# Kernel tuning notes

Measured on AMD Instinct MI355X. Metric: run time of the kernel, lower is better.

Reference implementation:

```python
import jax, jax.numpy as jnp
import numpy as np
from jax import lax

VOCAB, E, H = 32000, 256, 512
B, T = 64, 1024


def setup_inputs() -> dict:
    key = jax.random.key(0)
    ks = jax.random.split(key, 5)
    tokens = jax.random.randint(ks[0], (B, T), 0, VOCAB, dtype=jnp.int64 if jax.config.jax_enable_x64 else jnp.int32).astype(jnp.int32)
    emb_table = jax.random.normal(ks[1], (VOCAB, E), dtype=jnp.float32) * 0.02
    W_x = jax.random.normal(ks[2], (E, 4 * H), dtype=jnp.float32) * 0.02
    W_h = jax.random.normal(ks[3], (H, 4 * H), dtype=jnp.float32) * 0.02
    b = jnp.zeros((4 * H,), dtype=jnp.float32)
    h0 = jnp.zeros((B, H), dtype=jnp.float32)
    c0 = jnp.zeros((B, H), dtype=jnp.float32)
    return {"tokens": tokens, "h0": h0, "c0": c0, "emb_table": emb_table,
            "W_x": W_x, "W_h": W_h, "b": b}


def reference(tokens, h0, c0, emb_table, W_x, W_h, b):
    # Embedding lookup with mask_zero=True semantics: token 0 is padding.
    x = emb_table[tokens]                      # [B, T, E]
    mask = tokens != 0                         # [B, T]
    # Precompute input projections for all timesteps (same math, one GEMM).
    xz = jnp.einsum('bte,ef->btf', x, W_x) + b  # [B, T, 4H]

    def step(carry, inp):
        h, c = carry
        xzt, mt = inp                          # [B,4H], [B]
        z = xzt + h @ W_h                      # [B, 4H]
        i, f, g, o = jnp.split(z, 4, axis=-1)  # Keras gate order: i, f, c, o
        i = jax.nn.sigmoid(i)
        f = jax.nn.sigmoid(f)
        g = jnp.tanh(g)
        o = jax.nn.sigmoid(o)
        c_new = f * c + i * g
        h_new = o * jnp.tanh(c_new)
        m = mt[:, None]
        # Masked steps carry previous state/output (Keras masking behavior).
        h = jnp.where(m, h_new, h)
        c = jnp.where(m, c_new, c)
        return (h, c), h

    (h_T, c_T), outs = lax.scan(step, (h0, c0),
                                (xz.transpose(1, 0, 2), mask.T))
    return outs.transpose(1, 0, 2), h_T, c_T  # [B,T,H], [B,H], [B,H]
```

## Files before the change

kernel.cpp:

```cpp
#include <hip/hip_runtime.h>
#include <hip/hip_bf16.h>

#define B_ 64
#define T_ 1024
#define E_ 256
#define H_ 512
#define ZN_ 2048
#define NSLICE 64
#define KTX 8
#define KTH 16
#define KT_ (KTX + KTH)

typedef short bf16x8 __attribute__((ext_vector_type(8)));
typedef float f32x4 __attribute__((ext_vector_type(4)));
typedef int i32x4 __attribute__((ext_vector_type(4)));

union frag_u { i32x4 i; bf16x8 h; };

#define RAW_BAR() __builtin_amdgcn_s_barrier()
#define LGKM0() asm volatile("s_waitcnt lgkmcnt(0)" ::: "memory")
#define VM0() asm volatile("s_waitcnt vmcnt(0)" ::: "memory")

__device__ __forceinline__ short f2bf(float f) {
  union { float f; unsigned u; } v; v.f = f;
  unsigned r = v.u + 0x7fffu + ((v.u >> 16) & 1u);
  return (short)(r >> 16);
}
__device__ __forceinline__ float sigmoidf_(float x) { return 1.f / (1.f + __expf(-x)); }
__device__ __forceinline__ float tanhf_(float x) {
  x = fminf(10.f, fmaxf(-10.f, x));
  float e = __expf(2.f * x);
  return (e - 1.f) / (e + 1.f);
}

__device__ __forceinline__ i32x4 ld_sys(const void* p) {
  i32x4 r;
  asm volatile("global_load_dwordx4 %0, %1, off sc0 sc1" : "=v"(r) : "v"(p) : "memory");
  return r;
}
__device__ __forceinline__ void st_sys(void* p, i32x4 v) {
  asm volatile("global_store_dwordx4 %0, %1, off sc0 sc1" :: "v"(p), "v"(v) : "memory");
}
__device__ __forceinline__ int ld_sys_poll(const int* p) {
  int r;
  asm volatile("global_load_dword %0, %1, off sc0 sc1\n\ts_waitcnt vmcnt(0)"
               : "=v"(r) : "v"(p) : "memory");
  return r;
}
__device__ __forceinline__ void st_sys_i32(int* p, int v) {
  asm volatile("global_store_dword %0, %1, off sc0 sc1" :: "v"(p), "v"(v) : "memory");
}


__global__ void k_emb_cvt(const float* __restrict__ emb, short* __restrict__ dst, int n8) {
  int i = blockIdx.x * blockDim.x + threadIdx.x;
  if (i >= n8) return;
  const float4* s = (const float4*)emb;
  float4 a = s[2 * i], b = s[2 * i + 1];
  bf16x8 o;
  o[0] = f2bf(a.x); o[1] = f2bf(a.y); o[2] = f2bf(a.z); o[3] = f2bf(a.w);
  o[4] = f2bf(b.x); o[5] = f2bf(b.y); o[6] = f2bf(b.z); o[7] = f2bf(b.w);
  ((bf16x8*)dst)[i] = o;
}

__global__ void k_wfrag(const float* __restrict__ Wx, const float* __restrict__ Wh,
                        short* __restrict__ wf) {
  int tid = blockIdx.x * blockDim.x + threadIdx.x;
  if (tid >= NSLICE * 2 * KT_ * 64) return;
  int lane = tid & 63;
  int kt = (tid >> 6) % KT_;
  int nt = (tid >> 6) / KT_ % 2;
  int s = tid / (64 * KT_ * 2);
  int c16 = lane & 15, ksub = lane >> 4;
  int g = c16 & 3, hc = c16 >> 2;
  int zcol = g * H_ + s * 8 + nt * 4 + hc;
  int k0 = kt * 32 + ksub * 8;
  bf16x8 o;
#pragma unroll
  for (int i = 0; i < 8; ++i) {
    int k = k0 + i;
    float v = (k < E_) ? Wx[(size_t)k * ZN_ + zcol] : Wh[(size_t)(k - E_) * ZN_ + zcol];
    o[i] = f2bf(v);
  }
  ((bf16x8*)wf)[tid] = o;
}

__global__ void k_tok(const int* __restrict__ tok, int* __restrict__ tokT,
                      unsigned long long* __restrict__ mask) {
  int t = blockIdx.x * blockDim.x + threadIdx.x;
  if (t >= T_) return;
  unsigned long long m = 0ull;
  for (int b = 0; b < B_; ++b) {
    int tk = tok[b * T_ + t];
    tokT[t * B_ + b] = tk;
    if (tk != 0) m |= (1ull << b);
  }
  mask[t] = m;
}

__global__ void k_init(const float* __restrict__ h0, short* __restrict__ hbuf0,
                       int* __restrict__ flags) {
  int i = blockIdx.x * blockDim.x + threadIdx.x;
  if (i < 1024) flags[i] = 0;
  if (i >= B_ * H_) return;
  hbuf0[i] = f2bf(h0[i]);
}


__global__ __launch_bounds__(512, 2) void k_lstm(
    const int* __restrict__ tokT, const short* __restrict__ emb,
    const short* __restrict__ wf, const float* __restrict__ bias,
    const unsigned long long* __restrict__ maskv,
    short* __restrict__ hb0, short* __restrict__ hb1,
    const float* __restrict__ h0, const float* __restrict__ c0,
    float* __restrict__ out, int* __restrict__ flags)
{
  __shared__ __align__(16) short x_wf[2 * KTX * 64 * 8];
  __shared__ __align__(16) float hlocF[B_][8];
  __shared__ __align__(16) short hlocBF[B_][8];

  int s = blockIdx.x;
  int w = threadIdx.x >> 6, l = threadIdx.x & 63;
  int c16 = l & 15, ksub = l >> 4;
  int g = c16 & 3, hc = c16 >> 2;
  int base = l & ~3;
  int arow = w * 16 + c16;

  for (int idx = threadIdx.x; idx < 2 * KTX * 64; idx += 512) {
    int lane = idx & 63;
    int ktn = idx >> 6;
    int nt = ktn / KTX, kt = ktn % KTX;
    ((bf16x8*)x_wf)[idx] = ((const bf16x8*)wf)[(((size_t)(s * 2 + nt)) * KT_ + kt) * 64 + lane];
  }

  bf16x8 wreg0[KTH], wreg1[KTH];
  float zb0 = 0.f, zb1 = 0.f;
  float cst[2][4], hst[2][4];
  if (w < 4) {
    const bf16x8* b0 = (const bf16x8*)wf + (((size_t)(s * 2 + 0)) * KT_ + KTX) * 64 + l;
    const bf16x8* b1 = (const bf16x8*)wf + (((size_t)(s * 2 + 1)) * KT_ + KTX) * 64 + l;
#pragma unroll
    for (int kt = 0; kt < KTH; ++kt) { wreg0[kt] = b0[kt * 64]; wreg1[kt] = b1[kt * 64]; }
    zb0 = bias[g * H_ + s * 8 + 0 + hc];
    zb1 = bias[g * H_ + s * 8 + 4 + hc];
#pragma unroll
    for (int j = 0; j < 2; ++j) {
      int col = s * 8 + j * 4 + hc;
#pragma unroll
      for (int r = 0; r < 4; ++r) {
        int row = w * 16 + ksub * 4 + r;
        cst[j][r] = c0[row * H_ + col];
        hst[j][r] = h0[row * H_ + col];
      }
    }
  }
  LGKM0();
  RAW_BAR();

  f32x4 accx0 = {0.f, 0.f, 0.f, 0.f}, accx1 = {0.f, 0.f, 0.f, 0.f};
  auto compute_x = [&](int t) {
    int tk = tokT[t * B_ + arow];
    const bf16x8* ax = (const bf16x8*)emb + (size_t)tk * 32 + ksub;
    f32x4 a0 = {0.f, 0.f, 0.f, 0.f}, a1 = {0.f, 0.f, 0.f, 0.f};
#pragma unroll
    for (int kt = 0; kt < KTX; ++kt) {
      bf16x8 a = ax[kt * 4];
      a0 = __builtin_amdgcn_mfma_f32_16x16x32_bf16(a, ((const bf16x8*)x_wf)[(0 * KTX + kt) * 64 + l], a0, 0, 0, 0);
      a1 = __builtin_amdgcn_mfma_f32_16x16x32_bf16(a, ((const bf16x8*)x_wf)[(1 * KTX + kt) * 64 + l], a1, 0, 0, 0);
    }
    accx0 = a0; accx1 = a1;
  };

  if (w < 4) compute_x(0);

  for (int t = 0; t < T_; ++t) {
    const short* hr = (t & 1) ? hb1 : hb0;
    short* hw       = (t & 1) ? hb0 : hb1;

    if (w == 4 && t > 0) {
      for (;;) {
        int v = ld_sys_poll(flags + l * 16);
        if (__all(v >= t)) break;
        __builtin_amdgcn_s_sleep(1);
      }
    }
    RAW_BAR();

    if (w < 4) {
      const short* hbase = hr + arow * H_ + ksub * 8;
      frag_u hf[KTH];
#pragma unroll
      for (int kt = 0; kt < KTH; ++kt) hf[kt].i = ld_sys(hbase + kt * 32);
      VM0();
      __builtin_amdgcn_sched_barrier(0);

      f32x4 ac0 = accx0, ac1 = accx1;
#pragma unroll
      for (int kt = 0; kt < KTH; ++kt) {
        ac0 = __builtin_amdgcn_mfma_f32_16x16x32_bf16(hf[kt].h, wreg0[kt], ac0, 0, 0, 0);
        ac1 = __builtin_amdgcn_mfma_f32_16x16x32_bf16(hf[kt].h, wreg1[kt], ac1, 0, 0, 0);
      }

      unsigned long long mk = maskv[t];
#pragma unroll
      for (int j = 0; j < 2; ++j) {
        float zb = (j == 0) ? zb0 : zb1;
        int lc = j * 4 + hc;
        float act[4];
#pragma unroll
        for (int r = 0; r < 4; ++r) {
          float z = ((j == 0) ? ac0[r] : ac1[r]) + zb;
          act[r] = (g == 2) ? tanhf_(z) : sigmoidf_(z);
        }
#pragma unroll
        for (int r = 0; r < 4; ++r) {
          float fs = __shfl(act[r], base + 1);
          float gt = __shfl(act[r], base + 2);
          float os = __shfl(act[r], base + 3);
          if (g == 0) {
            int row = w * 16 + ksub * 4 + r;
            bool mm = (mk >> row) & 1ull;
            float cn = fs * cst[j][r] + act[r] * gt;
            float hn = os * tanhf_(cn);
            if (mm) { cst[j][r] = cn; hst[j][r] = hn; }
            hlocF[row][lc] = hst[j][r];
            hlocBF[row][lc] = f2bf(hst[j][r]);
          }
        }
      }
    }
    LGKM0();
    RAW_BAR();

    if (w == 4) {
      frag_u v; v.h = *(const bf16x8*)&hlocBF[l][0];
      st_sys(hw + l * H_ + s * 8, v.i);
      VM0();
      if (l == 0) st_sys_i32(flags + s * 16, t + 1);
    } else if (w == 5 || w == 6) {
      int p = (w - 5) * 64 + l;
      int row = p >> 1, half = p & 1;
      f32x4 v = *(const f32x4*)&hlocF[row][half * 4];
      __builtin_nontemporal_store(v, (f32x4*)(out + ((size_t)row * T_ + t) * H_ + s * 8 + half * 4));
    } else if (w < 4) {
      if (t == T_ - 1 && g == 0) {
#pragma unroll
        for (int j = 0; j < 2; ++j) {
          int col = s * 8 + j * 4 + hc;
#pragma unroll
          for (int r = 0; r < 4; ++r) {
            int row = w * 16 + ksub * 4 + r;
            out[(size_t)B_ * T_ * H_ + row * H_ + col] = hst[j][r];
            out[(size_t)B_ * T_ * H_ + B_ * H_ + row * H_ + col] = cst[j][r];
          }
        }
      }
      if (t + 1 < T_) compute_x(t + 1);
    }
  }
}


extern "C" void kernel_launch(void* const* d_in, const int* in_sizes, int n_in,
                              void* d_out, int out_size, void* d_ws, size_t ws_size,
                              hipStream_t stream) {
  (void)in_sizes; (void)n_in; (void)out_size; (void)ws_size;
  const int* tokens = (const int*)d_in[0];
  const float* h0 = (const float*)d_in[1];
  const float* c0 = (const float*)d_in[2];
  const float* emb = (const float*)d_in[3];
  const float* Wx = (const float*)d_in[4];
  const float* Wh = (const float*)d_in[5];
  const float* bias = (const float*)d_in[6];
  float* out = (float*)d_out;
  char* ws = (char*)d_ws;

  short* emb_bf = (short*)(ws);
  short* wf     = (short*)(ws + 16384000);
  unsigned long long* mask = (unsigned long long*)(ws + 19529728);
  int* tokT     = (int*)(ws + 19537920);
  short* hb0    = (short*)(ws + 19800064);
  short* hb1    = (short*)(ws + 19865600);
  int* flags    = (int*)(ws + 19931136);

  k_emb_cvt<<<(1024000 + 255) / 256, 256, 0, stream>>>(emb, emb_bf, 1024000);
  k_wfrag<<<(NSLICE * 2 * KT_ * 64 + 255) / 256, 256, 0, stream>>>(Wx, Wh, wf);
  k_tok<<<(T_ + 255) / 256, 256, 0, stream>>>(tokens, tokT, mask);
  k_init<<<(B_ * H_ + 255) / 256, 256, 0, stream>>>(h0, hb0, flags);

  k_lstm<<<NSLICE, 512, 0, stream>>>(tokT, emb_bf, wf, bias, mask,
                                     hb0, hb1, h0, c0, out, flags);
}
```

Baseline: 6.291 ms.

## Pack per-block step flags into bytes and publish h directly from compute waves

Compute waves now poll 16 packed dwords, each holding four per-block byte flags, instead of a dedicated wave polling 64 padded dword flags. That removes one block-wide barrier per timestep from the critical path. Each compute wave stores its own rows of the new h to global memory. A workgroup-scope atomic counter tells wave 4 when all four waves are done, and wave 4 then writes the block's byte flag. hlocF is double-buffered so the output-writing waves can lag safely. The risks are byte-flag wraparound across 256 steps and extra polling traffic from four waves per block.

```diff
diff --git a/kernel.cpp b/kernel.cpp
--- a/kernel.cpp
+++ b/kernel.cpp
@@ -47,8 +47,8 @@
                : "=v"(r) : "v"(p) : "memory");
   return r;
 }
-__device__ __forceinline__ void st_sys_i32(int* p, int v) {
-  asm volatile("global_store_dword %0, %1, off sc0 sc1" :: "v"(p), "v"(v) : "memory");
+__device__ __forceinline__ void st_sys_u8(char* p, int v) {
+  asm volatile("global_store_byte %0, %1, off sc0 sc1" :: "v"(p), "v"(v) : "memory");
 }
 
 
@@ -116,8 +116,9 @@
     float* __restrict__ out, int* __restrict__ flags)
 {
   __shared__ __align__(16) short x_wf[2 * KTX * 64 * 8];
-  __shared__ __align__(16) float hlocF[B_][8];
+  __shared__ __align__(16) float hlocF[2][B_][8];
   __shared__ __align__(16) short hlocBF[B_][8];
+  __shared__ int scnt;
 
   int s = blockIdx.x;
   int w = threadIdx.x >> 6, l = threadIdx.x & 63;
@@ -126,6 +127,8 @@
   int base = l & ~3;
   int arow = w * 16 + c16;
 
+  if (threadIdx.x == 0) scnt = 0;
+
   for (int idx = threadIdx.x; idx < 2 * KTX * 64; idx += 512) {
     int lane = idx & 63;
     int ktn = idx >> 6;
@@ -177,16 +180,15 @@
     const short* hr = (t & 1) ? hb1 : hb0;
     short* hw       = (t & 1) ? hb0 : hb1;
 
-    if (w == 4 && t > 0) {
-      for (;;) {
-        int v = ld_sys_poll(flags + l * 16);
-        if (__all(v >= t)) break;
-        __builtin_amdgcn_s_sleep(1);
-      }
-    }
-    RAW_BAR();
-
     if (w < 4) {
+      if (t > 0) {
+        int want = (t & 0xff) * 0x01010101;
+        for (;;) {
+          int v = ld_sys_poll(flags + (l & 15));
+          if (__all(v == want)) break;
+        }
+      }
+
       const short* hbase = hr + arow * H_ + ksub * 8;
       frag_u hf[KTH];
 #pragma unroll
@@ -223,39 +225,51 @@
             float cn = fs * cst[j][r] + act[r] * gt;
             float hn = os * tanhf_(cn);
             if (mm) { cst[j][r] = cn; hst[j][r] = hn; }
-            hlocF[row][lc] = hst[j][r];
+            hlocF[t & 1][row][lc] = hst[j][r];
             hlocBF[row][lc] = f2bf(hst[j][r]);
           }
         }
       }
-    }
-    LGKM0();
+
+      LGKM0();
+      if (l < 16) {
+        frag_u pv;
+        pv.h = *(const bf16x8*)&hlocBF[w * 16 + l][0];
+        st_sys(hw + (w * 16 + l) * H_ + s * 8, pv.i);
+      }
+      VM0();
+      if (l == 0)
+        __hip_atomic_fetch_add(&scnt, 1, __ATOMIC_RELAXED, __HIP_MEMORY_SCOPE_WORKGROUP);
+    } else if (w == 4) {
+      if (l == 0) {
+        int target = 4 * (t + 1);
+        while (__hip_atomic_load(&scnt, __ATOMIC_RELAXED, __HIP_MEMORY_SCOPE_WORKGROUP) < target) {}
+        st_sys_u8((char*)flags + s, (t + 1) & 0xff);
+      }
+    }
+
     RAW_BAR();
 
-    if (w == 4) {
-      frag_u v; v.h = *(const bf16x8*)&hlocBF[l][0];
-      st_sys(hw + l * H_ + s * 8, v.i);
-      VM0();
-      if (l == 0) st_sys_i32(flags + s * 16, t + 1);
-    } else if (w == 5 || w == 6) {
+    if (w == 5 || w == 6) {
       int p = (w - 5) * 64 + l;
       int row = p >> 1, half = p & 1;
-      f32x4 v = *(const f32x4*)&hlocF[row][half * 4];
+      f32x4 v = *(const f32x4*)&hlocF[t & 1][row][half * 4];
       __builtin_nontemporal_store(v, (f32x4*)(out + ((size_t)row * T_ + t) * H_ + s * 8 + half * 4));
-    } else if (w < 4) {
-      if (t == T_ - 1 && g == 0) {
-#pragma unroll
-        for (int j = 0; j < 2; ++j) {
-          int col = s * 8 + j * 4 + hc;
-#pragma unroll
-          for (int r = 0; r < 4; ++r) {
-            int row = w * 16 + ksub * 4 + r;
-            out[(size_t)B_ * T_ * H_ + row * H_ + col] = hst[j][r];
-            out[(size_t)B_ * T_ * H_ + B_ * H_ + row * H_ + col] = cst[j][r];
-          }
-        }
-      }
-      if (t + 1 < T_) compute_x(t + 1);
+    } else if (w < 4 && t + 1 < T_) {
+      compute_x(t + 1);
+    }
+  }
+
+  if (w < 4 && g == 0) {
+#pragma unroll
+    for (int j = 0; j < 2; ++j) {
+      int col = s * 8 + j * 4 + hc;
+#pragma unroll
+      for (int r = 0; r < 4; ++r) {
+        int row = w * 16 + ksub * 4 + r;
+        out[(size_t)B_ * T_ * H_ + row * H_ + col] = hst[j][r];
+        out[(size_t)B_ * T_ * H_ + B_ * H_ + row * H_ + col] = cst[j][r];
+      }
     }
   }
 }
```

Result: slower. 6.920 ms (+10.0%).

## Split LSTM grid into independent batch groups with per-group byte-flag sync

Applied to the files above, without the earlier changes.

Reorganizes the persistent LSTM so the 64 blocks form 4 batch groups of 16 rows, each spread across 16 hidden-column partitions. Cross-block synchronization now only spans the 16 blocks of a group, using byte flags packed into a single 16-byte line that one lane polls. Inside a block, workgroup barriers are replaced by LDS atomic counters, so compute, h publication and output stores can proceed without full-block barriers. The aim is to cut global barrier latency per timestep, at the cost of more complex intra-block ordering and byte flags that wrap modulo 256.

```diff
diff --git a/kernel.cpp b/kernel.cpp
--- a/kernel.cpp
+++ b/kernel.cpp
@@ -6,7 +6,8 @@
 #define E_ 256
 #define H_ 512
 #define ZN_ 2048
-#define NSLICE 64
+#define NG 4
+#define NP 16
 #define KTX 8
 #define KTH 16
 #define KT_ (KTX + KTH)
@@ -17,7 +18,6 @@
 
 union frag_u { i32x4 i; bf16x8 h; };
 
-#define RAW_BAR() __builtin_amdgcn_s_barrier()
 #define LGKM0() asm volatile("s_waitcnt lgkmcnt(0)" ::: "memory")
 #define VM0() asm volatile("s_waitcnt vmcnt(0)" ::: "memory")
 
@@ -38,17 +38,17 @@
   asm volatile("global_load_dwordx4 %0, %1, off sc0 sc1" : "=v"(r) : "v"(p) : "memory");
   return r;
 }
+__device__ __forceinline__ i32x4 ld_sys16_poll(const void* p) {
+  i32x4 r;
+  asm volatile("global_load_dwordx4 %0, %1, off sc0 sc1\n\ts_waitcnt vmcnt(0)"
+               : "=v"(r) : "v"(p) : "memory");
+  return r;
+}
 __device__ __forceinline__ void st_sys(void* p, i32x4 v) {
   asm volatile("global_store_dwordx4 %0, %1, off sc0 sc1" :: "v"(p), "v"(v) : "memory");
 }
-__device__ __forceinline__ int ld_sys_poll(const int* p) {
-  int r;
-  asm volatile("global_load_dword %0, %1, off sc0 sc1\n\ts_waitcnt vmcnt(0)"
-               : "=v"(r) : "v"(p) : "memory");
-  return r;
-}
-__device__ __forceinline__ void st_sys_i32(int* p, int v) {
-  asm volatile("global_store_dword %0, %1, off sc0 sc1" :: "v"(p), "v"(v) : "memory");
+__device__ __forceinline__ void st_sys_u8(char* p, int v) {
+  asm volatile("global_store_byte %0, %1, off sc0 sc1" :: "v"(p), "v"(v) : "memory");
 }
 
 
@@ -66,14 +66,14 @@
 __global__ void k_wfrag(const float* __restrict__ Wx, const float* __restrict__ Wh,
                         short* __restrict__ wf) {
   int tid = blockIdx.x * blockDim.x + threadIdx.x;
-  if (tid >= NSLICE * 2 * KT_ * 64) return;
+  if (tid >= NP * 8 * KT_ * 64) return;
   int lane = tid & 63;
   int kt = (tid >> 6) % KT_;
-  int nt = (tid >> 6) / KT_ % 2;
-  int s = tid / (64 * KT_ * 2);
+  int n = (tid >> 6) / KT_ % 8;
+  int p = tid / (64 * KT_ * 8);
   int c16 = lane & 15, ksub = lane >> 4;
-  int g = c16 & 3, hc = c16 >> 2;
-  int zcol = g * H_ + s * 8 + nt * 4 + hc;
+  int gate = c16 & 3, hc = c16 >> 2;
+  int zcol = gate * H_ + p * 32 + n * 4 + hc;
   int k0 = kt * 32 + ksub * 8;
   bf16x8 o;
 #pragma unroll
@@ -98,99 +98,93 @@
   mask[t] = m;
 }
 
-__global__ void k_init(const float* __restrict__ h0, short* __restrict__ hbuf0,
+__global__ void k_init(const float* __restrict__ h0, short* __restrict__ hx,
                        int* __restrict__ flags) {
   int i = blockIdx.x * blockDim.x + threadIdx.x;
   if (i < 1024) flags[i] = 0;
   if (i >= B_ * H_) return;
-  hbuf0[i] = f2bf(h0[i]);
-}
-
-
-__global__ __launch_bounds__(512, 2) void k_lstm(
+  int b = i >> 9, c = i & 511;
+  int g = b >> 4, r = b & 15;
+  hx[((size_t)(0 * NG + g) * 16 + r) * H_ + c] = f2bf(h0[i]);
+}
+
+
+__global__ __launch_bounds__(384, 2) void k_lstm(
     const int* __restrict__ tokT, const short* __restrict__ emb,
     const short* __restrict__ wf, const float* __restrict__ bias,
     const unsigned long long* __restrict__ maskv,
-    short* __restrict__ hb0, short* __restrict__ hb1,
+    short* __restrict__ hx,
     const float* __restrict__ h0, const float* __restrict__ c0,
     float* __restrict__ out, int* __restrict__ flags)
 {
-  __shared__ __align__(16) short x_wf[2 * KTX * 64 * 8];
-  __shared__ __align__(16) float hlocF[B_][8];
-  __shared__ __align__(16) short hlocBF[B_][8];
-
-  int s = blockIdx.x;
-  int w = threadIdx.x >> 6, l = threadIdx.x & 63;
-  int c16 = l & 15, ksub = l >> 4;
-  int g = c16 & 3, hc = c16 >> 2;
-  int base = l & ~3;
-  int arow = w * 16 + c16;
-
-  for (int idx = threadIdx.x; idx < 2 * KTX * 64; idx += 512) {
-    int lane = idx & 63;
-    int ktn = idx >> 6;
-    int nt = ktn / KTX, kt = ktn % KTX;
-    ((bf16x8*)x_wf)[idx] = ((const bf16x8*)wf)[(((size_t)(s * 2 + nt)) * KT_ + kt) * 64 + lane];
+  __shared__ __align__(16) short x_wf[8 * KTX * 64 * 8];
+  __shared__ __align__(16) float hlocF[2][16][32];
+  __shared__ __align__(16) short hlocBF[16][32];
+  __shared__ int scnt, gcnt, ocnt;
+
+  const int sb = blockIdx.x, g = sb >> 4, p = sb & 15;
+  const int w = threadIdx.x >> 6, l = threadIdx.x & 63;
+  const int c16 = l & 15, ksub = l >> 4;
+  const int gate = c16 & 3, hc = c16 >> 2;
+  const int base = l & ~3;
+
+  if (threadIdx.x == 0) { scnt = 0; gcnt = 0; ocnt = 0; }
+
+  for (int idx = threadIdx.x; idx < 8 * KTX * 64; idx += 384) {
+    int lane = idx & 63, ktn = idx >> 6;
+    int n = ktn >> 3, kt = ktn & 7;
+    ((bf16x8*)x_wf)[idx] = ((const bf16x8*)wf)[(((size_t)p * 8 + n) * KT_ + kt) * 64 + lane];
   }
 
   bf16x8 wreg0[KTH], wreg1[KTH];
-  float zb0 = 0.f, zb1 = 0.f;
-  float cst[2][4], hst[2][4];
+  float zb0 = 0.f, zb1 = 0.f, cst[2][4], hst[2][4];
   if (w < 4) {
-    const bf16x8* b0 = (const bf16x8*)wf + (((size_t)(s * 2 + 0)) * KT_ + KTX) * 64 + l;
-    const bf16x8* b1 = (const bf16x8*)wf + (((size_t)(s * 2 + 1)) * KT_ + KTX) * 64 + l;
+    const bf16x8* b0 = (const bf16x8*)wf + (((size_t)p * 8 + 2 * w + 0) * KT_ + KTX) * 64 + l;
+    const bf16x8* b1 = (const bf16x8*)wf + (((size_t)p * 8 + 2 * w + 1) * KT_ + KTX) * 64 + l;
 #pragma unroll
     for (int kt = 0; kt < KTH; ++kt) { wreg0[kt] = b0[kt * 64]; wreg1[kt] = b1[kt * 64]; }
-    zb0 = bias[g * H_ + s * 8 + 0 + hc];
-    zb1 = bias[g * H_ + s * 8 + 4 + hc];
+    zb0 = bias[gate * H_ + p * 32 + (2 * w + 0) * 4 + hc];
+    zb1 = bias[gate * H_ + p * 32 + (2 * w + 1) * 4 + hc];
 #pragma unroll
     for (int j = 0; j < 2; ++j) {
-      int col = s * 8 + j * 4 + hc;
+      int col = p * 32 + (2 * w + j) * 4 + hc;
 #pragma unroll
       for (int r = 0; r < 4; ++r) {
-        int row = w * 16 + ksub * 4 + r;
+        int row = g * 16 + ksub * 4 + r;
         cst[j][r] = c0[row * H_ + col];
         hst[j][r] = h0[row * H_ + col];
       }
     }
   }
-  LGKM0();
-  RAW_BAR();
+  __syncthreads();
 
   f32x4 accx0 = {0.f, 0.f, 0.f, 0.f}, accx1 = {0.f, 0.f, 0.f, 0.f};
   auto compute_x = [&](int t) {
-    int tk = tokT[t * B_ + arow];
-    const bf16x8* ax = (const bf16x8*)emb + (size_t)tk * 32 + ksub;
+    int tk = tokT[t * B_ + g * 16 + c16];
+    const short* ax = emb + (size_t)tk * 256 + ksub * 8;
     f32x4 a0 = {0.f, 0.f, 0.f, 0.f}, a1 = {0.f, 0.f, 0.f, 0.f};
 #pragma unroll
     for (int kt = 0; kt < KTX; ++kt) {
-      bf16x8 a = ax[kt * 4];
-      a0 = __builtin_amdgcn_mfma_f32_16x16x32_bf16(a, ((const bf16x8*)x_wf)[(0 * KTX + kt) * 64 + l], a0, 0, 0, 0);
-      a1 = __builtin_amdgcn_mfma_f32_16x16x32_bf16(a, ((const bf16x8*)x_wf)[(1 * KTX + kt) * 64 + l], a1, 0, 0, 0);
+      bf16x8 a = *(const bf16x8*)(ax + kt * 32);
+      a0 = __builtin_amdgcn_mfma_f32_16x16x32_bf16(a, ((const bf16x8*)x_wf)[((2 * w + 0) * KTX + kt) * 64 + l], a0, 0, 0, 0);
+      a1 = __builtin_amdgcn_mfma_f32_16x16x32_bf16(a, ((const bf16x8*)x_wf)[((2 * w + 1) * KTX + kt) * 64 + l], a1, 0, 0, 0);
     }
     accx0 = a0; accx1 = a1;
   };
-
   if (w < 4) compute_x(0);
 
+  char* flagline = (char*)flags + g * 256;
+
   for (int t = 0; t < T_; ++t) {
-    const short* hr = (t & 1) ? hb1 : hb0;
-    short* hw       = (t & 1) ? hb0 : hb1;
-
-    if (w == 4 && t > 0) {
-      for (;;) {
-        int v = ld_sys_poll(flags + l * 16);
-        if (__all(v >= t)) break;
-        __builtin_amdgcn_s_sleep(1);
-      }
-    }
-    RAW_BAR();
-
+    int par = t & 1;
     if (w < 4) {
-      const short* hbase = hr + arow * H_ + ksub * 8;
+      if (t > 0)
+        while (__hip_atomic_load(&gcnt, __ATOMIC_ACQUIRE, __HIP_MEMORY_SCOPE_WORKGROUP) < t) {}
+
+      const short* hr = hx + (((size_t)par * NG + g) * 16 + c16) * H_ + ksub * 8;
       frag_u hf[KTH];
 #pragma unroll
-      for (int kt = 0; kt < KTH; ++kt) hf[kt].i = ld_sys(hbase + kt * 32);
+      for (int kt = 0; kt < KTH; ++kt) hf[kt].i = ld_sys(hr + kt * 32);
       VM0();
       __builtin_amdgcn_sched_barrier(0);
 
@@ -201,61 +195,82 @@
         ac1 = __builtin_amdgcn_mfma_f32_16x16x32_bf16(hf[kt].h, wreg1[kt], ac1, 0, 0, 0);
       }
 
-      unsigned long long mk = maskv[t];
+      while (__hip_atomic_load(&ocnt, __ATOMIC_ACQUIRE, __HIP_MEMORY_SCOPE_WORKGROUP) < t - 1) {}
+
+      unsigned long long mk = maskv[t] >> (g * 16);
 #pragma unroll
       for (int j = 0; j < 2; ++j) {
-        float zb = (j == 0) ? zb0 : zb1;
-        int lc = j * 4 + hc;
+        float zb = j ? zb1 : zb0;
+        int lc = (2 * w + j) * 4 + hc;
         float act[4];
 #pragma unroll
         for (int r = 0; r < 4; ++r) {
-          float z = ((j == 0) ? ac0[r] : ac1[r]) + zb;
-          act[r] = (g == 2) ? tanhf_(z) : sigmoidf_(z);
+          float z = (j ? ac1[r] : ac0[r]) + zb;
+          act[r] = (gate == 2) ? tanhf_(z) : sigmoidf_(z);
         }
 #pragma unroll
         for (int r = 0; r < 4; ++r) {
           float fs = __shfl(act[r], base + 1);
           float gt = __shfl(act[r], base + 2);
           float os = __shfl(act[r], base + 3);
-          if (g == 0) {
-            int row = w * 16 + ksub * 4 + r;
-            bool mm = (mk >> row) & 1ull;
+          if (gate == 0) {
+            int row16 = ksub * 4 + r;
+            bool mm = (mk >> row16) & 1ull;
             float cn = fs * cst[j][r] + act[r] * gt;
             float hn = os * tanhf_(cn);
             if (mm) { cst[j][r] = cn; hst[j][r] = hn; }
-            hlocF[row][lc] = hst[j][r];
-            hlocBF[row][lc] = f2bf(hst[j][r]);
+            hlocF[par][row16][lc] = hst[j][r];
+            hlocBF[row16][lc] = f2bf(hst[j][r]);
           }
         }
       }
+
+      LGKM0();
+      if (l < 16) {
+        frag_u pv; pv.h = *(const bf16x8*)&hlocBF[l][w * 8];
+        st_sys(hx + (((size_t)(1 - par) * NG + g) * 16 + l) * H_ + p * 32 + w * 8, pv.i);
+      }
+      VM0();
+      if (l == 0)
+        __hip_atomic_fetch_add(&scnt, 1, __ATOMIC_RELEASE, __HIP_MEMORY_SCOPE_WORKGROUP);
+
+      if (t + 1 < T_) compute_x(t + 1);
+    } else if (w == 4) {
+      if (l == 0) {
+        while (__hip_atomic_load(&scnt, __ATOMIC_ACQUIRE, __HIP_MEMORY_SCOPE_WORKGROUP) < 4 * (t + 1)) {}
+        st_sys_u8(flagline + p, (t + 1) & 0xff);
+        int want = ((t + 1) & 0xff) * 0x01010101;
+        for (;;) {
+          i32x4 f = ld_sys16_poll(flagline);
+          if (f[0] == want && f[1] == want && f[2] == want && f[3] == want) break;
+          __builtin_amdgcn_s_sleep(1);
+        }
+        __hip_atomic_store(&gcnt, t + 1, __ATOMIC_RELEASE, __HIP_MEMORY_SCOPE_WORKGROUP);
+      }
+    } else {
+      while (__hip_atomic_load(&scnt, __ATOMIC_ACQUIRE, __HIP_MEMORY_SCOPE_WORKGROUP) < 4 * (t + 1)) {}
+      int row16 = l >> 2, q = l & 3;
+      f32x4 v0 = *(const f32x4*)&hlocF[par][row16][q * 4];
+      f32x4 v1 = *(const f32x4*)&hlocF[par][row16][16 + q * 4];
+      LGKM0();
+      if (l == 0)
+        __hip_atomic_store(&ocnt, t + 1, __ATOMIC_RELEASE, __HIP_MEMORY_SCOPE_WORKGROUP);
+      float* ob = out + (((size_t)(g * 16 + row16)) * T_ + t) * H_ + p * 32;
+      __builtin_nontemporal_store(v0, (f32x4*)(ob + q * 4));
+      __builtin_nontemporal_store(v1, (f32x4*)(ob + 16 + q * 4));
     }
-    LGKM0();
-    RAW_BAR();
-
-    if (w == 4) {
-      frag_u v; v.h = *(const bf16x8*)&hlocBF[l][0];
-      st_sys(hw + l * H_ + s * 8, v.i);
-      VM0();
-      if (l == 0) st_sys_i32(flags + s * 16, t + 1);
-    } else if (w == 5 || w == 6) {
-      int p = (w - 5) * 64 + l;
-      int row = p >> 1, half = p & 1;
-      f32x4 v = *(const f32x4*)&hlocF[row][half * 4];
-      __builtin_nontemporal_store(v, (f32x4*)(out + ((size_t)row * T_ + t) * H_ + s * 8 + half * 4));
-    } else if (w < 4) {
-      if (t == T_ - 1 && g == 0) {
-#pragma unroll
-        for (int j = 0; j < 2; ++j) {
-          int col = s * 8 + j * 4 + hc;
-#pragma unroll
-          for (int r = 0; r < 4; ++r) {
-            int row = w * 16 + ksub * 4 + r;
-            out[(size_t)B_ * T_ * H_ + row * H_ + col] = hst[j][r];
-            out[(size_t)B_ * T_ * H_ + B_ * H_ + row * H_ + col] = cst[j][r];
-          }
-        }
-      }
-      if (t + 1 < T_) compute_x(t + 1);
+  }
+
+  if (w < 4 && gate == 0) {
+#pragma unroll
+    for (int j = 0; j < 2; ++j) {
+      int col = p * 32 + (2 * w + j) * 4 + hc;
+#pragma unroll
+      for (int r = 0; r < 4; ++r) {
+        int row = g * 16 + ksub * 4 + r;
+        out[(size_t)B_ * T_ * H_ + row * H_ + col] = hst[j][r];
+        out[(size_t)B_ * T_ * H_ + B_ * H_ + row * H_ + col] = cst[j][r];
+      }
     }
   }
 }
@@ -279,15 +294,14 @@
   short* wf     = (short*)(ws + 16384000);
   unsigned long long* mask = (unsigned long long*)(ws + 19529728);
   int* tokT     = (int*)(ws + 19537920);
-  short* hb0    = (short*)(ws + 19800064);
-  short* hb1    = (short*)(ws + 19865600);
+  short* hx     = (short*)(ws + 19800064);
   int* flags    = (int*)(ws + 19931136);
 
   k_emb_cvt<<<(1024000 + 255) / 256, 256, 0, stream>>>(emb, emb_bf, 1024000);
-  k_wfrag<<<(NSLICE * 2 * KT_ * 64 + 255) / 256, 256, 0, stream>>>(Wx, Wh, wf);
+  k_wfrag<<<(NP * 8 * KT_ * 64 + 255) / 256, 256, 0, stream>>>(Wx, Wh, wf);
   k_tok<<<(T_ + 255) / 256, 256, 0, stream>>>(tokens, tokT, mask);
-  k_init<<<(B_ * H_ + 255) / 256, 256, 0, stream>>>(h0, hb0, flags);
-
-  k_lstm<<<NSLICE, 512, 0, stream>>>(tokT, emb_bf, wf, bias, mask,
-                                     hb0, hb1, h0, c0, out, flags);
-}
+  k_init<<<(B_ * H_ + 255) / 256, 256, 0, stream>>>(h0, hx, flags);
+
+  k_lstm<<<NG * NP, 384, 0, stream>>>(tokT, emb_bf, wf, bias, mask,
+                                      hx, h0, c0, out, flags);
+}
```

Result: no change. 6.400 ms (+1.7%).

## Replace block barriers with per-wave global tags and LDS counters in LSTM recurrence

Applied to the files above, without the earlier changes.

The four compute waves now each poll a 256-entry per-wave tag array with one 16-byte load per lane, without sleeping. Each wave publishes its own 16 rows of h to global memory and then sets its own tag, which removes the dedicated publisher wave and both block-wide barriers per timestep. The fp32 output writes move to two decoupled waves that sync through LDS atomic counters, with hlocF double-buffered so output stores stay off the critical path. Block size drops from 512 to 384 threads, and the block now depends on busy-spinning in LDS and finer-grained global flag traffic.

```diff
diff --git a/kernel.cpp b/kernel.cpp
--- a/kernel.cpp
+++ b/kernel.cpp
@@ -20,6 +20,7 @@
 #define RAW_BAR() __builtin_amdgcn_s_barrier()
 #define LGKM0() asm volatile("s_waitcnt lgkmcnt(0)" ::: "memory")
 #define VM0() asm volatile("s_waitcnt vmcnt(0)" ::: "memory")
+#define SCHED_BAR() __builtin_amdgcn_sched_barrier(0)
 
 __device__ __forceinline__ short f2bf(float f) {
   union { float f; unsigned u; } v; v.f = f;
@@ -38,14 +39,14 @@
   asm volatile("global_load_dwordx4 %0, %1, off sc0 sc1" : "=v"(r) : "v"(p) : "memory");
   return r;
 }
+__device__ __forceinline__ i32x4 ld_sys16_poll(const void* p) {
+  i32x4 r;
+  asm volatile("global_load_dwordx4 %0, %1, off sc0 sc1\n\ts_waitcnt vmcnt(0)"
+               : "=v"(r) : "v"(p) : "memory");
+  return r;
+}
 __device__ __forceinline__ void st_sys(void* p, i32x4 v) {
   asm volatile("global_store_dwordx4 %0, %1, off sc0 sc1" :: "v"(p), "v"(v) : "memory");
-}
-__device__ __forceinline__ int ld_sys_poll(const int* p) {
-  int r;
-  asm volatile("global_load_dword %0, %1, off sc0 sc1\n\ts_waitcnt vmcnt(0)"
-               : "=v"(r) : "v"(p) : "memory");
-  return r;
 }
 __device__ __forceinline__ void st_sys_i32(int* p, int v) {
   asm volatile("global_store_dword %0, %1, off sc0 sc1" :: "v"(p), "v"(v) : "memory");
@@ -107,17 +108,18 @@
 }
 
 
-__global__ __launch_bounds__(512, 2) void k_lstm(
+__global__ __launch_bounds__(384, 1) void k_lstm(
     const int* __restrict__ tokT, const short* __restrict__ emb,
     const short* __restrict__ wf, const float* __restrict__ bias,
     const unsigned long long* __restrict__ maskv,
     short* __restrict__ hb0, short* __restrict__ hb1,
     const float* __restrict__ h0, const float* __restrict__ c0,
-    float* __restrict__ out, int* __restrict__ flags)
+    float* __restrict__ out, int* __restrict__ tags)
 {
   __shared__ __align__(16) short x_wf[2 * KTX * 64 * 8];
-  __shared__ __align__(16) float hlocF[B_][8];
+  __shared__ __align__(16) float hlocF[2][B_][8];
   __shared__ __align__(16) short hlocBF[B_][8];
+  __shared__ int scnt, ocnt;
 
   int s = blockIdx.x;
   int w = threadIdx.x >> 6, l = threadIdx.x & 63;
@@ -126,7 +128,9 @@
   int base = l & ~3;
   int arow = w * 16 + c16;
 
-  for (int idx = threadIdx.x; idx < 2 * KTX * 64; idx += 512) {
+  if (threadIdx.x == 0) { scnt = 0; ocnt = 0; }
+
+  for (int idx = threadIdx.x; idx < 2 * KTX * 64; idx += 384) {
     int lane = idx & 63;
     int ktn = idx >> 6;
     int nt = ktn / KTX, kt = ktn % KTX;
@@ -173,26 +177,25 @@
 
   if (w < 4) compute_x(0);
 
-  for (int t = 0; t < T_; ++t) {
-    const short* hr = (t & 1) ? hb1 : hb0;
-    short* hw       = (t & 1) ? hb0 : hb1;
-
-    if (w == 4 && t > 0) {
-      for (;;) {
-        int v = ld_sys_poll(flags + l * 16);
-        if (__all(v >= t)) break;
-        __builtin_amdgcn_s_sleep(1);
-      }
-    }
-    RAW_BAR();
-
-    if (w < 4) {
+  if (w < 4) {
+    for (int t = 0; t < T_; ++t) {
+      int par = t & 1;
+      const short* hr = (t & 1) ? hb1 : hb0;
+      short* hw       = (t & 1) ? hb0 : hb1;
+
+      if (t > 0) {
+        for (;;) {
+          i32x4 tg = ld_sys16_poll(tags + l * 4);
+          if (__all(tg[0] >= t && tg[1] >= t && tg[2] >= t && tg[3] >= t)) break;
+        }
+      }
+
       const short* hbase = hr + arow * H_ + ksub * 8;
       frag_u hf[KTH];
 #pragma unroll
       for (int kt = 0; kt < KTH; ++kt) hf[kt].i = ld_sys(hbase + kt * 32);
       VM0();
-      __builtin_amdgcn_sched_barrier(0);
+      SCHED_BAR();
 
       f32x4 ac0 = accx0, ac1 = accx1;
 #pragma unroll
@@ -200,6 +203,8 @@
         ac0 = __builtin_amdgcn_mfma_f32_16x16x32_bf16(hf[kt].h, wreg0[kt], ac0, 0, 0, 0);
         ac1 = __builtin_amdgcn_mfma_f32_16x16x32_bf16(hf[kt].h, wreg1[kt], ac1, 0, 0, 0);
       }
+
+      while (__hip_atomic_load(&ocnt, __ATOMIC_ACQUIRE, __HIP_MEMORY_SCOPE_WORKGROUP) < 2 * (t - 1)) {}
 
       unsigned long long mk = maskv[t];
 #pragma unroll
@@ -223,26 +228,21 @@
             float cn = fs * cst[j][r] + act[r] * gt;
             float hn = os * tanhf_(cn);
             if (mm) { cst[j][r] = cn; hst[j][r] = hn; }
-            hlocF[row][lc] = hst[j][r];
+            hlocF[par][row][lc] = hst[j][r];
             hlocBF[row][lc] = f2bf(hst[j][r]);
           }
         }
       }
-    }
-    LGKM0();
-    RAW_BAR();
-
-    if (w == 4) {
-      frag_u v; v.h = *(const bf16x8*)&hlocBF[l][0];
-      st_sys(hw + l * H_ + s * 8, v.i);
-      VM0();
-      if (l == 0) st_sys_i32(flags + s * 16, t + 1);
-    } else if (w == 5 || w == 6) {
-      int p = (w - 5) * 64 + l;
-      int row = p >> 1, half = p & 1;
-      f32x4 v = *(const f32x4*)&hlocF[row][half * 4];
-      __builtin_nontemporal_store(v, (f32x4*)(out + ((size_t)row * T_ + t) * H_ + s * 8 + half * 4));
-    } else if (w < 4) {
+      LGKM0();
+      SCHED_BAR();
+
+      if (l == 0)
+        __hip_atomic_fetch_add(&scnt, 1, __ATOMIC_RELEASE, __HIP_MEMORY_SCOPE_WORKGROUP);
+
+      if (l < 16) {
+        frag_u pv; pv.h = *(const bf16x8*)&hlocBF[w * 16 + l][0];
+        st_sys(hw + (w * 16 + l) * H_ + s * 8, pv.i);
+      }
       if (t == T_ - 1 && g == 0) {
 #pragma unroll
         for (int j = 0; j < 2; ++j) {
@@ -255,7 +255,21 @@
           }
         }
       }
+      VM0();
+      if (l == 0) st_sys_i32(tags + (s * 4 + w), t + 1);
+
       if (t + 1 < T_) compute_x(t + 1);
+    }
+  } else {
+    for (int t = 0; t < T_; ++t) {
+      int par = t & 1;
+      while (__hip_atomic_load(&scnt, __ATOMIC_ACQUIRE, __HIP_MEMORY_SCOPE_WORKGROUP) < 4 * (t + 1)) {}
+      int row = (w - 4) * 32 + (l >> 1), half = l & 1;
+      f32x4 v = *(const f32x4*)&hlocF[par][row][half * 4];
+      LGKM0();
+      if (l == 0)
+        __hip_atomic_fetch_add(&ocnt, 1, __ATOMIC_RELEASE, __HIP_MEMORY_SCOPE_WORKGROUP);
+      __builtin_nontemporal_store(v, (f32x4*)(out + ((size_t)row * T_ + t) * H_ + s * 8 + half * 4));
     }
   }
 }
@@ -281,13 +295,13 @@
   int* tokT     = (int*)(ws + 19537920);
   short* hb0    = (short*)(ws + 19800064);
   short* hb1    = (short*)(ws + 19865600);
-  int* flags    = (int*)(ws + 19931136);
+  int* tags     = (int*)(ws + 19931136);
 
   k_emb_cvt<<<(1024000 + 255) / 256, 256, 0, stream>>>(emb, emb_bf, 1024000);
   k_wfrag<<<(NSLICE * 2 * KT_ * 64 + 255) / 256, 256, 0, stream>>>(Wx, Wh, wf);
   k_tok<<<(T_ + 255) / 256, 256, 0, stream>>>(tokens, tokT, mask);
-  k_init<<<(B_ * H_ + 255) / 256, 256, 0, stream>>>(h0, hb0, flags);
-
-  k_lstm<<<NSLICE, 512, 0, stream>>>(tokT, emb_bf, wf, bias, mask,
-                                     hb0, hb1, h0, c0, out, flags);
-}
+  k_init<<<(B_ * H_ + 255) / 256, 256, 0, stream>>>(h0, hb0, tags);
+
+  k_lstm<<<NSLICE, 384, 0, stream>>>(tokT, emb_bf, wf, bias, mask,
+                                     hb0, hb1, h0, c0, out, tags);
+}
```

Result: slower. 6.563 ms (+4.3%).
